# Kernel optimization log

Measured on AMD Instinct MI355X. Metric: run time of the kernel, lower is better.

Reference implementation:

```python
import jax, jax.numpy as jnp
import numpy as np

N = 4096      # number of projected gaussians
W = 512       # screen width
H = 512       # screen height
TL = 64       # tile_length
NT = W // TL  # tiles per axis (8) -> NT*NT = 64 tiles


def setup_inputs() -> dict:
    key = jax.random.key(0)
    k1, k2, k3, k4, k5 = jax.random.split(key, 5)
    xy = jax.random.uniform(k1, (N, 2), dtype=jnp.float32) * W          # screen positions
    depth = jax.random.uniform(k2, (N, 1), dtype=jnp.float32) * 10.0 + 0.1
    pos2d = jnp.concatenate([xy, depth], axis=1)                        # [N,3] = (x, y, depth)
    A = jax.random.normal(k3, (N, 2, 2), dtype=jnp.float32)
    cov2d = 9.0 * jnp.einsum('nij,nkj->nik', A, A) + jnp.eye(2, dtype=jnp.float32)  # PSD, ~3px sigma
    opacity = jax.random.uniform(k4, (N,), dtype=jnp.float32)
    color = jax.random.uniform(k5, (N, 3), dtype=jnp.float32)           # SH-evaluated RGB (pre +0.5 clamp)
    return {"pos2d": pos2d, "cov2d": cov2d, "opacity": opacity, "color": color}


def _render(pos2d, cov2d, opacity, color):
    # Global depth sort == per-tile argsort of the masked subset (order is preserved).
    order = jnp.argsort(pos2d[:, 2])
    pos = pos2d[order]
    cov = cov2d[order]
    op = opacity[order]
    col = jnp.clip(color[order] + 0.5, 0.0, None)  # color = clamp(eval_sh + 0.5, min=0)

    a, b = cov[:, 0, 0], cov[:, 0, 1]
    c, d = cov[:, 1, 0], cov[:, 1, 1]
    trace = a + d
    det = a * d - b * c
    term2 = 0.5 * jnp.sqrt(jnp.clip(trace * trace - 4.0 * det, 0.0, None))
    radius = 3.0 * jnp.sqrt(jnp.maximum(0.5 * trace - term2, 0.5 * trace + term2))

    inv_det = 1.0 / det
    ia = d * inv_det
    ib = -b * inv_det
    ic = -c * inv_det
    id_ = a * inv_det
    px, py = pos[:, 0], pos[:, 1]

    def tile_fn(tid):
        tx = tid // NT
        ty = tid % NT
        left = (tx * TL).astype(jnp.float32)
        top = (ty * TL).astype(jnp.float32)
        xs = left + jnp.arange(TL, dtype=jnp.float32)  # pixel x coords of tile rows
        ys = top + jnp.arange(TL, dtype=jnp.float32)   # pixel y coords of tile cols
        # gaussian's 3-sigma circle overlaps tile rect -> included in this tile
        inmask = ((px + radius >= left) & (px - radius < left + TL) &
                  (py + radius >= top) & (py - radius < top + TL))
        dx = xs[:, None, None] - px[None, None, :]  # [TL,1,K]
        dy = ys[None, :, None] - py[None, None, :]  # [1,TL,K]
        # mahalanobis distance: d^T Sigma^{-1} d  -> [TL,TL,K]
        q = ia * dx * dx + (ib + ic) * dx * dy + id_ * dy * dy
        prob = jnp.exp(-0.5 * q)
        alpha = jnp.where(inmask, jnp.clip(op * prob, 0.01, 0.99), 0.0)  # excluded -> alpha 0
        # transmittance: cumprod of (1 - alpha) shifted by one (front-to-back)
        ones = jnp.ones((TL, TL, 1), dtype=alpha.dtype)
        weight = jnp.cumprod(jnp.concatenate([ones, 1.0 - alpha[:, :, :-1]], axis=2), axis=2)
        return jnp.einsum('xyk,kc->xyc', alpha * weight, col)  # [TL,TL,3]

    tiles = jax.lax.map(tile_fn, jnp.arange(NT * NT))  # [NT*NT, TL, TL, 3]
    img = tiles.reshape(NT, NT, TL, TL, 3).transpose(0, 2, 1, 3, 4).reshape(W, H, 3)
    return img


def reference(pos2d, cov2d, opacity, color):
    return _render(pos2d, cov2d, opacity, color)
```

## Files before the change

kernel.cpp:

```cpp
#include <hip/hip_runtime.h>


#define N_G    4096
#define W_IMG  512
#define TL_    64
#define NTILES 64
#define LOG2E  1.44269504088896340736f

typedef float v2f __attribute__((ext_vector_type(2)));


__global__ __launch_bounds__(256)
void gs_preprocess(const float* __restrict__ pos2d,
                   const float* __restrict__ cov2d,
                   const float* __restrict__ opacity,
                   const float* __restrict__ color,
                   float4* __restrict__ a4,
                   float4* __restrict__ b4,
                   float* __restrict__ c1,
                   unsigned long long* __restrict__ tmask) {
    __shared__ __align__(16) float s_depth[N_G];
    const int t = threadIdx.x;

    for (int k = t; k < N_G; k += 256)
        s_depth[k] = pos2d[k * 3 + 2];
    __syncthreads();

    const int g = t >> 5;
    const int s = t & 31;
    const int i = blockIdx.x * 8 + g;
    const float di = s_depth[i];

    const float4* s_d4 = (const float4*)s_depth;
    int rank = 0;
    #pragma unroll 8
    for (int k = 0; k < 32; ++k) {
        const int j4 = s + 32 * k;
        const float4 d = s_d4[j4];
        const int j = 4 * j4;
        rank += (d.x < di) || (d.x == di && (j + 0) < i);
        rank += (d.y < di) || (d.y == di && (j + 1) < i);
        rank += (d.z < di) || (d.z == di && (j + 2) < i);
        rank += (d.w < di) || (d.w == di && (j + 3) < i);
    }
    rank += __shfl_xor(rank, 1);
    rank += __shfl_xor(rank, 2);
    rank += __shfl_xor(rank, 4);
    rank += __shfl_xor(rank, 8);
    rank += __shfl_xor(rank, 16);

    if (s == 0) {
        const float px = pos2d[i * 3 + 0];
        const float py = pos2d[i * 3 + 1];
        const float a = cov2d[i * 4 + 0];
        const float b = cov2d[i * 4 + 1];
        const float c = cov2d[i * 4 + 2];
        const float d = cov2d[i * 4 + 3];

        const float trace = a + d;
        const float det = a * d - b * c;
        const float tmp = trace * trace - 4.0f * det;
        const float term2 = 0.5f * sqrtf(fmaxf(tmp, 0.0f));
        const float radius = 3.0f * sqrtf(fmaxf(0.5f * trace - term2, 0.5f * trace + term2));
        const float inv_det = 1.0f / det;
        const float ia  = d * inv_det;
        const float ibc = (-b * inv_det) + (-c * inv_det);
        const float idd = a * inv_det;

        const float op = opacity[i];
        const float cr = fmaxf(color[i * 3 + 0] + 0.5f, 0.0f);
        const float cg = fmaxf(color[i * 3 + 1] + 0.5f, 0.0f);
        const float cb = fmaxf(color[i * 3 + 2] + 0.5f, 0.0f);

        unsigned int xm = 0, ym = 0;
        #pragma unroll
        for (int tc = 0; tc < 8; ++tc) {
            const float lo = (float)(tc * TL_);
            if ((px + radius >= lo) && (px - radius < lo + (float)TL_)) xm |= 1u << tc;
            if ((py + radius >= lo) && (py - radius < lo + (float)TL_)) ym |= 1u << tc;
        }
        unsigned long long m = 0ull;
        #pragma unroll
        for (int tc = 0; tc < 8; ++tc)
            if (xm & (1u << tc)) m |= (unsigned long long)ym << (8 * tc);

        a4[rank] = make_float4(px, py, -0.5f * ia * LOG2E, -0.5f * ibc * LOG2E);
        b4[rank] = make_float4(-0.5f * idd * LOG2E, __log2f(op), cr, cg);
        c1[rank] = cb;
        tmask[rank] = m;
    }
}

__global__ __launch_bounds__(512, 4)
void gs_render(const float4* __restrict__ a4,
               const float4* __restrict__ b4,
               const float* __restrict__ c1,
               const unsigned long long* __restrict__ tmask,
               float* __restrict__ out) {
    __shared__ unsigned short s_list[N_G];
    __shared__ int s_wcnt[8];
    __shared__ __align__(16) float4 s_wa[8][64];
    __shared__ __align__(16) float4 s_wb[8][64];
    __shared__ float s_wc[8][64];
    __shared__ __align__(16) float4 s_m[4][512];

    const int id = blockIdx.x;
    const int sub  = id >> 6;
    const int tile = ((id & 63) * 21 + sub * 11) & 63;
    const int tx = tile >> 3;
    const int ty = tile & 7;
    const int t = threadIdx.x;
    const int wave = t >> 6;
    const int lane = t & 63;

    unsigned int bits = 0;
    int wcnt = 0;
    #pragma unroll 4
    for (int it = 0; it < 8; ++it) {
        const int g = wave * 512 + it * 64 + lane;
        const bool m = (tmask[g] >> tile) & 1ull;
        bits |= (m ? 1u : 0u) << it;
        wcnt += __popcll(__ballot(m));
    }
    if (lane == 0) s_wcnt[wave] = wcnt;
    __syncthreads();
    int total = 0, base = 0;
    #pragma unroll
    for (int w = 0; w < 8; ++w) {
        const int c = s_wcnt[w];
        total += c;
        if (w < wave) base += c;
    }
    #pragma unroll 4
    for (int it = 0; it < 8; ++it) {
        const bool m = (bits >> it) & 1u;
        const unsigned long long bal = __ballot(m);
        const int prefix = __popcll(bal & ((1ULL << lane) - 1ULL));
        if (m) s_list[base + prefix] = (unsigned short)(wave * 512 + it * 64 + lane);
        base += __popcll(bal);
    }
    __syncthreads();

    const int s0 = (wave * total) >> 3;
    const int s1 = ((wave + 1) * total) >> 3;

    const int X0 = tx * TL_ + sub * 8;
    const int Y  = ty * TL_ + lane;
    const float fY = (float)Y;

    const v2f fX0 = {(float)(X0 + 0), (float)(X0 + 1)};
    const v2f fX1 = {(float)(X0 + 2), (float)(X0 + 3)};
    const v2f fX2 = {(float)(X0 + 4), (float)(X0 + 5)};
    const v2f fX3 = {(float)(X0 + 6), (float)(X0 + 7)};

    v2f R0 = {0.f, 0.f}, R1 = R0, R2 = R0, R3 = R0;
    v2f G0 = R0, G1 = R0, G2 = R0, G3 = R0;
    v2f B0 = R0, B1 = R0, B2 = R0, B3 = R0;
    v2f T0 = {1.f, 1.f}, T1 = T0, T2 = T0, T3 = T0;

    float4* const wa = s_wa[wave];
    float4* const wb = s_wb[wave];
    float*  const wc = s_wc[wave];

    float4 va, vb;
    float vc = 0.f;
    if (s0 + lane < s1) {
        const int g = s_list[s0 + lane];
        va = a4[g]; vb = b4[g]; vc = c1[g];
    }

    for (int c = s0; c < s1; c += 64) {
        const int n = min(64, s1 - c);
        if (lane < n) { wa[lane] = va; wb[lane] = vb; wc[lane] = vc; }
        const int cn = c + 64;
        if (cn + lane < s1) {
            const int g = s_list[cn + lane];
            va = a4[g]; vb = b4[g]; vc = c1[g];
        }
        #pragma unroll 4
        for (int k = 0; k < n; ++k) {
            const float4 A  = wa[k];
            const float4 Bv = wb[k];
            const float cbv = wc[k];

            const float dy   = fY - A.y;
            const float qbdy = A.w * dy;
            const float bse  = Bv.x * dy * dy + Bv.y;
            const v2f az2 = {A.z, A.z};
            const v2f ax2 = {A.x, A.x};
            const v2f qb2 = {qbdy, qbdy};
            const v2f bs2 = {bse, bse};
            const v2f lo2 = {0.01f, 0.01f};
            const v2f hi2 = {0.99f, 0.99f};
            const v2f cr2 = {Bv.z, Bv.z};
            const v2f cg2 = {Bv.w, Bv.w};
            const v2f cb2 = {cbv, cbv};
#define PX_PAIR(FXP, Tp, Rp, Gp, Bp)                                          \
            {                                                                 \
                const v2f dx = FXP - ax2;                                     \
                v2f q = __builtin_elementwise_fma(az2, dx, qb2);              \
                q = __builtin_elementwise_fma(q, dx, bs2);                    \
                v2f e;                                                        \
                e.x = exp2f(q.x); e.y = exp2f(q.y);                           \
                v2f al;                                                       \
                al.x = __builtin_amdgcn_fmed3f(e.x, lo2.x, hi2.x);            \
                al.y = __builtin_amdgcn_fmed3f(e.y, lo2.y, hi2.y);            \
                const v2f w_ = al * Tp;                                       \
                Rp = __builtin_elementwise_fma(w_, cr2, Rp);                  \
                Gp = __builtin_elementwise_fma(w_, cg2, Gp);                  \
                Bp = __builtin_elementwise_fma(w_, cb2, Bp);                  \
                Tp = Tp - w_;                                                 \
            }
            PX_PAIR(fX0, T0, R0, G0, B0)
            PX_PAIR(fX1, T1, R1, G1, B1)
            PX_PAIR(fX2, T2, R2, G2, B2)
            PX_PAIR(fX3, T3, R3, G3, B3)
#undef PX_PAIR
        }
    }

#define PUBLISH(buf)                                                          \
    {                                                                         \
        (buf)[0 * 64 + lane] = make_float4(R0.x, G0.x, B0.x, T0.x);           \
        (buf)[1 * 64 + lane] = make_float4(R0.y, G0.y, B0.y, T0.y);           \
        (buf)[2 * 64 + lane] = make_float4(R1.x, G1.x, B1.x, T1.x);           \
        (buf)[3 * 64 + lane] = make_float4(R1.y, G1.y, B1.y, T1.y);           \
        (buf)[4 * 64 + lane] = make_float4(R2.x, G2.x, B2.x, T2.x);           \
        (buf)[5 * 64 + lane] = make_float4(R2.y, G2.y, B2.y, T2.y);           \
        (buf)[6 * 64 + lane] = make_float4(R3.x, G3.x, B3.x, T3.x);           \
        (buf)[7 * 64 + lane] = make_float4(R3.y, G3.y, B3.y, T3.y);           \
    }
#define COMPOSE(buf)                                                          \
    {                                                                         \
        _Pragma("unroll")                                                     \
        for (int j = 0; j < 4; ++j) {                                         \
            const float4 m0 = (buf)[(2 * j + 0) * 64 + lane];                 \
            const float4 m1 = (buf)[(2 * j + 1) * 64 + lane];                 \
            const v2f mr = {m0.x, m1.x};                                      \
            const v2f mg = {m0.y, m1.y};                                      \
            const v2f mb = {m0.z, m1.z};                                      \
            const v2f mt = {m0.w, m1.w};                                      \
            v2f* Rj = j == 0 ? &R0 : j == 1 ? &R1 : j == 2 ? &R2 : &R3;       \
            v2f* Gj = j == 0 ? &G0 : j == 1 ? &G1 : j == 2 ? &G2 : &G3;       \
            v2f* Bj = j == 0 ? &B0 : j == 1 ? &B1 : j == 2 ? &B2 : &B3;       \
            v2f* Tj = j == 0 ? &T0 : j == 1 ? &T1 : j == 2 ? &T2 : &T3;       \
            *Rj = __builtin_elementwise_fma(*Tj, mr, *Rj);                    \
            *Gj = __builtin_elementwise_fma(*Tj, mg, *Gj);                    \
            *Bj = __builtin_elementwise_fma(*Tj, mb, *Bj);                    \
            *Tj = *Tj * mt;                                                   \
        }                                                                     \
    }

    if (wave & 1) PUBLISH(s_m[wave >> 1]);
    __syncthreads();
    if (!(wave & 1)) COMPOSE(s_m[wave >> 1]);
    if (wave == 2) PUBLISH(s_m[1]);
    if (wave == 6) PUBLISH(s_m[3]);
    __syncthreads();
    if (wave == 0) COMPOSE(s_m[1]);
    if (wave == 4) COMPOSE(s_m[3]);
    if (wave == 4) PUBLISH(s_m[3]);
    __syncthreads();
    if (wave == 0) {
        COMPOSE(s_m[3]);
#define OUT_PX(i, tv, rv, gv, bv)                                             \
        {                                                                     \
            const int o = ((X0 + (i)) * W_IMG + Y) * 3;                       \
            out[o + 0] = rv;                                                  \
            out[o + 1] = gv;                                                  \
            out[o + 2] = bv;                                                  \
        }
        OUT_PX(0, T0.x, R0.x, G0.x, B0.x)
        OUT_PX(1, T0.y, R0.y, G0.y, B0.y)
        OUT_PX(2, T1.x, R1.x, G1.x, B1.x)
        OUT_PX(3, T1.y, R1.y, G1.y, B1.y)
        OUT_PX(4, T2.x, R2.x, G2.x, B2.x)
        OUT_PX(5, T2.y, R2.y, G2.y, B2.y)
        OUT_PX(6, T3.x, R3.x, G3.x, B3.x)
        OUT_PX(7, T3.y, R3.y, G3.y, B3.y)
#undef OUT_PX
    }
#undef PUBLISH
#undef COMPOSE
}

extern "C" void kernel_launch(void* const* d_in, const int* in_sizes, int n_in,
                              void* d_out, int out_size, void* d_ws, size_t ws_size,
                              hipStream_t stream) {
    const float* pos2d   = (const float*)d_in[0];
    const float* cov2d   = (const float*)d_in[1];
    const float* opacity = (const float*)d_in[2];
    const float* color   = (const float*)d_in[3];
    float* out = (float*)d_out;

    char* ws = (char*)d_ws;
    float4* a4 = (float4*)(ws);
    float4* b4 = (float4*)(ws + 65536);
    float*  c1 = (float*)(ws + 131072);
    unsigned long long* tm = (unsigned long long*)(ws + 147456);

    gs_preprocess<<<N_G / 8, 256, 0, stream>>>(pos2d, cov2d, opacity, color,
                                               a4, b4, c1, tm);
    gs_render<<<NTILES * 8, 512, 0, stream>>>(a4, b4, c1, tm, out);
}
```

Baseline: 33.59 us.

## Schedule render blocks by per-tile gaussian count for load balancing

Preprocess now atomically counts the gaussians overlapping each tile. Every render block ranks the tiles by that count and remaps its block id so the heaviest tiles are dispatched first, with the sub-blocks interleaved to spread load. The aim is to cut the tail imbalance from uneven tile workloads. The cost is an extra memset launch, global atomics in preprocess, and a 64x64 ranking step repeated in every render block.

```diff
diff --git a/kernel.cpp b/kernel.cpp
--- a/kernel.cpp
+++ b/kernel.cpp
@@ -18,7 +18,8 @@
                    float4* __restrict__ a4,
                    float4* __restrict__ b4,
                    float* __restrict__ c1,
-                   unsigned long long* __restrict__ tmask) {
+                   unsigned long long* __restrict__ tmask,
+                   int* __restrict__ cnt) {
     __shared__ __align__(16) float s_depth[N_G];
     const int t = threadIdx.x;
 
@@ -88,6 +89,13 @@
         b4[rank] = make_float4(-0.5f * idd * LOG2E, __log2f(op), cr, cg);
         c1[rank] = cb;
         tmask[rank] = m;
+
+        unsigned long long mm = m;
+        while (mm) {
+            const int bit = (int)__builtin_ctzll(mm);
+            atomicAdd(&cnt[bit], 1);
+            mm &= mm - 1ull;
+        }
     }
 }
 
@@ -96,22 +104,42 @@
                const float4* __restrict__ b4,
                const float* __restrict__ c1,
                const unsigned long long* __restrict__ tmask,
+               const int* __restrict__ cnt,
                float* __restrict__ out) {
     __shared__ unsigned short s_list[N_G];
     __shared__ int s_wcnt[8];
+    __shared__ int s_cnt[64];
+    __shared__ unsigned char s_sorted[64];
     __shared__ __align__(16) float4 s_wa[8][64];
     __shared__ __align__(16) float4 s_wb[8][64];
     __shared__ float s_wc[8][64];
     __shared__ __align__(16) float4 s_m[4][512];
 
     const int id = blockIdx.x;
-    const int sub  = id >> 6;
-    const int tile = ((id & 63) * 21 + sub * 11) & 63;
-    const int tx = tile >> 3;
-    const int ty = tile & 7;
     const int t = threadIdx.x;
     const int wave = t >> 6;
     const int lane = t & 63;
+
+    if (t < 64) s_cnt[t] = cnt[t];
+    __syncthreads();
+    if (t < 64) {
+        const int c = s_cnt[t];
+        int r = 0;
+        #pragma unroll
+        for (int j = 0; j < 64; ++j) {
+            const int cj = s_cnt[j];
+            r += (cj > c) || (cj == c && j < t);
+        }
+        s_sorted[r] = (unsigned char)t;
+    }
+    __syncthreads();
+    const int slot = id & 63;
+    const int sub  = id >> 6;
+    const int rr = (sub < 4) ? ((slot + sub * 16) & 63)
+                             : (63 - ((slot + (sub - 4) * 16) & 63));
+    const int tile = s_sorted[rr];
+    const int tx = tile >> 3;
+    const int ty = tile & 7;
 
     unsigned int bits = 0;
     int wcnt = 0;
@@ -263,21 +291,21 @@
     __syncthreads();
     if (wave == 0) {
         COMPOSE(s_m[3]);
-#define OUT_PX(i, tv, rv, gv, bv)                                             \
+#define OUT_PX(i, rv, gv, bv)                                                 \
         {                                                                     \
             const int o = ((X0 + (i)) * W_IMG + Y) * 3;                       \
             out[o + 0] = rv;                                                  \
             out[o + 1] = gv;                                                  \
             out[o + 2] = bv;                                                  \
         }
-        OUT_PX(0, T0.x, R0.x, G0.x, B0.x)
-        OUT_PX(1, T0.y, R0.y, G0.y, B0.y)
-        OUT_PX(2, T1.x, R1.x, G1.x, B1.x)
-        OUT_PX(3, T1.y, R1.y, G1.y, B1.y)
-        OUT_PX(4, T2.x, R2.x, G2.x, B2.x)
-        OUT_PX(5, T2.y, R2.y, G2.y, B2.y)
-        OUT_PX(6, T3.x, R3.x, G3.x, B3.x)
-        OUT_PX(7, T3.y, R3.y, G3.y, B3.y)
+        OUT_PX(0, R0.x, G0.x, B0.x)
+        OUT_PX(1, R0.y, G0.y, B0.y)
+        OUT_PX(2, R1.x, G1.x, B1.x)
+        OUT_PX(3, R1.y, G1.y, B1.y)
+        OUT_PX(4, R2.x, G2.x, B2.x)
+        OUT_PX(5, R2.y, G2.y, B2.y)
+        OUT_PX(6, R3.x, G3.x, B3.x)
+        OUT_PX(7, R3.y, G3.y, B3.y)
 #undef OUT_PX
     }
 #undef PUBLISH
@@ -298,8 +326,10 @@
     float4* b4 = (float4*)(ws + 65536);
     float*  c1 = (float*)(ws + 131072);
     unsigned long long* tm = (unsigned long long*)(ws + 147456);
-
+    int*    ct = (int*)(ws + 180224);
+
+    hipMemsetAsync(ct, 0, 64 * sizeof(int), stream);
     gs_preprocess<<<N_G / 8, 256, 0, stream>>>(pos2d, cov2d, opacity, color,
-                                               a4, b4, c1, tm);
-    gs_render<<<NTILES * 8, 512, 0, stream>>>(a4, b4, c1, tm, out);
+                                               a4, b4, c1, tm, ct);
+    gs_render<<<NTILES * 8, 512, 0, stream>>>(a4, b4, c1, tm, ct, out);
 }
```

Result: slower. 72.43 us (+115.6%).

## Fuse preprocessing into render kernel with per-tile local depth sort

Applied to the files above, without the earlier changes.

Removes the separate preprocess kernel. Each render block now computes radii and tile overlap for all gaussians, sorts only the gaussians that touch its tile by a local rank count in shared memory, and builds its parameter arrays in LDS. The render loop reads those directly, replacing the chunked global-load double-buffering, and the final merge is serialized through two shared buffers. This saves a kernel launch and the global round-trip, but every block redundantly reads all 4096 gaussians, caps the per-tile list at 1024 entries, and adds more barriers to the merge.

```diff
diff --git a/kernel.cpp b/kernel.cpp
--- a/kernel.cpp
+++ b/kernel.cpp
@@ -5,120 +5,59 @@
 #define W_IMG  512
 #define TL_    64
 #define NTILES 64
+#define MAXG   1024
 #define LOG2E  1.44269504088896340736f
 
 typedef float v2f __attribute__((ext_vector_type(2)));
 
-
-__global__ __launch_bounds__(256)
-void gs_preprocess(const float* __restrict__ pos2d,
-                   const float* __restrict__ cov2d,
-                   const float* __restrict__ opacity,
-                   const float* __restrict__ color,
-                   float4* __restrict__ a4,
-                   float4* __restrict__ b4,
-                   float* __restrict__ c1,
-                   unsigned long long* __restrict__ tmask) {
-    __shared__ __align__(16) float s_depth[N_G];
-    const int t = threadIdx.x;
-
-    for (int k = t; k < N_G; k += 256)
-        s_depth[k] = pos2d[k * 3 + 2];
-    __syncthreads();
-
-    const int g = t >> 5;
-    const int s = t & 31;
-    const int i = blockIdx.x * 8 + g;
-    const float di = s_depth[i];
-
-    const float4* s_d4 = (const float4*)s_depth;
-    int rank = 0;
-    #pragma unroll 8
-    for (int k = 0; k < 32; ++k) {
-        const int j4 = s + 32 * k;
-        const float4 d = s_d4[j4];
-        const int j = 4 * j4;
-        rank += (d.x < di) || (d.x == di && (j + 0) < i);
-        rank += (d.y < di) || (d.y == di && (j + 1) < i);
-        rank += (d.z < di) || (d.z == di && (j + 2) < i);
-        rank += (d.w < di) || (d.w == di && (j + 3) < i);
-    }
-    rank += __shfl_xor(rank, 1);
-    rank += __shfl_xor(rank, 2);
-    rank += __shfl_xor(rank, 4);
-    rank += __shfl_xor(rank, 8);
-    rank += __shfl_xor(rank, 16);
-
-    if (s == 0) {
-        const float px = pos2d[i * 3 + 0];
-        const float py = pos2d[i * 3 + 1];
-        const float a = cov2d[i * 4 + 0];
-        const float b = cov2d[i * 4 + 1];
-        const float c = cov2d[i * 4 + 2];
-        const float d = cov2d[i * 4 + 3];
-
-        const float trace = a + d;
-        const float det = a * d - b * c;
-        const float tmp = trace * trace - 4.0f * det;
-        const float term2 = 0.5f * sqrtf(fmaxf(tmp, 0.0f));
-        const float radius = 3.0f * sqrtf(fmaxf(0.5f * trace - term2, 0.5f * trace + term2));
-        const float inv_det = 1.0f / det;
-        const float ia  = d * inv_det;
-        const float ibc = (-b * inv_det) + (-c * inv_det);
-        const float idd = a * inv_det;
-
-        const float op = opacity[i];
-        const float cr = fmaxf(color[i * 3 + 0] + 0.5f, 0.0f);
-        const float cg = fmaxf(color[i * 3 + 1] + 0.5f, 0.0f);
-        const float cb = fmaxf(color[i * 3 + 2] + 0.5f, 0.0f);
-
-        unsigned int xm = 0, ym = 0;
-        #pragma unroll
-        for (int tc = 0; tc < 8; ++tc) {
-            const float lo = (float)(tc * TL_);
-            if ((px + radius >= lo) && (px - radius < lo + (float)TL_)) xm |= 1u << tc;
-            if ((py + radius >= lo) && (py - radius < lo + (float)TL_)) ym |= 1u << tc;
-        }
-        unsigned long long m = 0ull;
-        #pragma unroll
-        for (int tc = 0; tc < 8; ++tc)
-            if (xm & (1u << tc)) m |= (unsigned long long)ym << (8 * tc);
-
-        a4[rank] = make_float4(px, py, -0.5f * ia * LOG2E, -0.5f * ibc * LOG2E);
-        b4[rank] = make_float4(-0.5f * idd * LOG2E, __log2f(op), cr, cg);
-        c1[rank] = cb;
-        tmask[rank] = m;
-    }
-}
+struct PreScratch {
+    float dep[MAXG];
+    unsigned short srv[MAXG];
+};
 
 __global__ __launch_bounds__(512, 4)
-void gs_render(const float4* __restrict__ a4,
-               const float4* __restrict__ b4,
-               const float* __restrict__ c1,
-               const unsigned long long* __restrict__ tmask,
-               float* __restrict__ out) {
-    __shared__ unsigned short s_list[N_G];
+void gs_fused(const float* __restrict__ pos2d,
+              const float* __restrict__ cov2d,
+              const float* __restrict__ opacity,
+              const float* __restrict__ color,
+              float* __restrict__ out) {
+    __shared__ __align__(16) float4 sA[MAXG];
+    __shared__ __align__(16) float4 sB[MAXG];
+    __shared__ float sC[MAXG];
     __shared__ int s_wcnt[8];
-    __shared__ __align__(16) float4 s_wa[8][64];
-    __shared__ __align__(16) float4 s_wb[8][64];
-    __shared__ float s_wc[8][64];
-    __shared__ __align__(16) float4 s_m[4][512];
+    __shared__ union {
+        PreScratch pre;
+        __align__(16) float4 m[2][512];
+    } su;
 
     const int id = blockIdx.x;
     const int sub  = id >> 6;
     const int tile = ((id & 63) * 21 + sub * 11) & 63;
     const int tx = tile >> 3;
     const int ty = tile & 7;
+    const float left = (float)(tx * TL_);
+    const float top  = (float)(ty * TL_);
     const int t = threadIdx.x;
     const int wave = t >> 6;
     const int lane = t & 63;
 
     unsigned int bits = 0;
     int wcnt = 0;
-    #pragma unroll 4
+    float dep8[8];
+    #pragma unroll
     for (int it = 0; it < 8; ++it) {
         const int g = wave * 512 + it * 64 + lane;
-        const bool m = (tmask[g] >> tile) & 1ull;
+        const float px = pos2d[g * 3 + 0];
+        const float py = pos2d[g * 3 + 1];
+        dep8[it] = pos2d[g * 3 + 2];
+        const float4 cv = ((const float4*)cov2d)[g];
+        const float trace = cv.x + cv.w;
+        const float det = cv.x * cv.w - cv.y * cv.z;
+        const float tmp = trace * trace - 4.0f * det;
+        const float term2 = 0.5f * sqrtf(fmaxf(tmp, 0.0f));
+        const float radius = 3.0f * sqrtf(fmaxf(0.5f * trace - term2, 0.5f * trace + term2));
+        const bool m = (px + radius >= left) && (px - radius < left + (float)TL_) &&
+                       (py + radius >= top)  && (py - radius < top  + (float)TL_);
         bits |= (m ? 1u : 0u) << it;
         wcnt += __popcll(__ballot(m));
     }
@@ -131,18 +70,63 @@
         total += c;
         if (w < wave) base += c;
     }
-    #pragma unroll 4
+    const int totalc = min(total, MAXG);
+
+    #pragma unroll
     for (int it = 0; it < 8; ++it) {
         const bool m = (bits >> it) & 1u;
         const unsigned long long bal = __ballot(m);
         const int prefix = __popcll(bal & ((1ULL << lane) - 1ULL));
-        if (m) s_list[base + prefix] = (unsigned short)(wave * 512 + it * 64 + lane);
+        const int pos = base + prefix;
+        if (m && pos < MAXG) {
+            su.pre.srv[pos] = (unsigned short)(wave * 512 + it * 64 + lane);
+            su.pre.dep[pos] = dep8[it];
+        }
         base += __popcll(bal);
     }
-    __syncthreads();
-
-    const int s0 = (wave * total) >> 3;
-    const int s1 = ((wave + 1) * total) >> 3;
+    if (t < 8) {
+        const int p = totalc + t;
+        if (p < MAXG) su.pre.dep[p] = 1e30f;
+    }
+    __syncthreads();
+
+    if (t < totalc) {
+        const float dt = su.pre.dep[t];
+        const float4* d4 = (const float4*)su.pre.dep;
+        int rank = 0;
+        const int n4 = (totalc + 3) >> 2;
+        for (int j4 = 0; j4 < n4; ++j4) {
+            const float4 d = d4[j4];
+            const int j = 4 * j4;
+            rank += (d.x < dt) || (d.x == dt && (j + 0) < t);
+            rank += (d.y < dt) || (d.y == dt && (j + 1) < t);
+            rank += (d.z < dt) || (d.z == dt && (j + 2) < t);
+            rank += (d.w < dt) || (d.w == dt && (j + 3) < t);
+        }
+        const int g = su.pre.srv[t];
+        const float px = pos2d[g * 3 + 0];
+        const float py = pos2d[g * 3 + 1];
+        const float a = cov2d[g * 4 + 0];
+        const float b = cov2d[g * 4 + 1];
+        const float c = cov2d[g * 4 + 2];
+        const float d = cov2d[g * 4 + 3];
+        const float det = a * d - b * c;
+        const float inv_det = 1.0f / det;
+        const float ia  = d * inv_det;
+        const float ibc = (-b * inv_det) + (-c * inv_det);
+        const float idd = a * inv_det;
+        const float op = opacity[g];
+        const float cr = fmaxf(color[g * 3 + 0] + 0.5f, 0.0f);
+        const float cg = fmaxf(color[g * 3 + 1] + 0.5f, 0.0f);
+        const float cb = fmaxf(color[g * 3 + 2] + 0.5f, 0.0f);
+        sA[rank] = make_float4(px, py, -0.5f * ia * LOG2E, -0.5f * ibc * LOG2E);
+        sB[rank] = make_float4(-0.5f * idd * LOG2E, __log2f(op), cr, cg);
+        sC[rank] = cb;
+    }
+    __syncthreads();
+
+    const int s0 = (wave * totalc) >> 3;
+    const int s1 = ((wave + 1) * totalc) >> 3;
 
     const int X0 = tx * TL_ + sub * 8;
     const int Y  = ty * TL_ + lane;
@@ -158,65 +142,45 @@
     v2f B0 = R0, B1 = R0, B2 = R0, B3 = R0;
     v2f T0 = {1.f, 1.f}, T1 = T0, T2 = T0, T3 = T0;
 
-    float4* const wa = s_wa[wave];
-    float4* const wb = s_wb[wave];
-    float*  const wc = s_wc[wave];
-
-    float4 va, vb;
-    float vc = 0.f;
-    if (s0 + lane < s1) {
-        const int g = s_list[s0 + lane];
-        va = a4[g]; vb = b4[g]; vc = c1[g];
-    }
-
-    for (int c = s0; c < s1; c += 64) {
-        const int n = min(64, s1 - c);
-        if (lane < n) { wa[lane] = va; wb[lane] = vb; wc[lane] = vc; }
-        const int cn = c + 64;
-        if (cn + lane < s1) {
-            const int g = s_list[cn + lane];
-            va = a4[g]; vb = b4[g]; vc = c1[g];
-        }
-        #pragma unroll 4
-        for (int k = 0; k < n; ++k) {
-            const float4 A  = wa[k];
-            const float4 Bv = wb[k];
-            const float cbv = wc[k];
-
-            const float dy   = fY - A.y;
-            const float qbdy = A.w * dy;
-            const float bse  = Bv.x * dy * dy + Bv.y;
-            const v2f az2 = {A.z, A.z};
-            const v2f ax2 = {A.x, A.x};
-            const v2f qb2 = {qbdy, qbdy};
-            const v2f bs2 = {bse, bse};
-            const v2f lo2 = {0.01f, 0.01f};
-            const v2f hi2 = {0.99f, 0.99f};
-            const v2f cr2 = {Bv.z, Bv.z};
-            const v2f cg2 = {Bv.w, Bv.w};
-            const v2f cb2 = {cbv, cbv};
+    #pragma unroll 4
+    for (int k = s0; k < s1; ++k) {
+        const float4 A  = sA[k];
+        const float4 Bv = sB[k];
+        const float cbv = sC[k];
+
+        const float dy   = fY - A.y;
+        const float qbdy = A.w * dy;
+        const float bse  = Bv.x * dy * dy + Bv.y;
+        const v2f az2 = {A.z, A.z};
+        const v2f ax2 = {A.x, A.x};
+        const v2f qb2 = {qbdy, qbdy};
+        const v2f bs2 = {bse, bse};
+        const v2f lo2 = {0.01f, 0.01f};
+        const v2f hi2 = {0.99f, 0.99f};
+        const v2f cr2 = {Bv.z, Bv.z};
+        const v2f cg2 = {Bv.w, Bv.w};
+        const v2f cb2 = {cbv, cbv};
 #define PX_PAIR(FXP, Tp, Rp, Gp, Bp)                                          \
-            {                                                                 \
-                const v2f dx = FXP - ax2;                                     \
-                v2f q = __builtin_elementwise_fma(az2, dx, qb2);              \
-                q = __builtin_elementwise_fma(q, dx, bs2);                    \
-                v2f e;                                                        \
-                e.x = exp2f(q.x); e.y = exp2f(q.y);                           \
-                v2f al;                                                       \
-                al.x = __builtin_amdgcn_fmed3f(e.x, lo2.x, hi2.x);            \
-                al.y = __builtin_amdgcn_fmed3f(e.y, lo2.y, hi2.y);            \
-                const v2f w_ = al * Tp;                                       \
-                Rp = __builtin_elementwise_fma(w_, cr2, Rp);                  \
-                Gp = __builtin_elementwise_fma(w_, cg2, Gp);                  \
-                Bp = __builtin_elementwise_fma(w_, cb2, Bp);                  \
-                Tp = Tp - w_;                                                 \
-            }
-            PX_PAIR(fX0, T0, R0, G0, B0)
-            PX_PAIR(fX1, T1, R1, G1, B1)
-            PX_PAIR(fX2, T2, R2, G2, B2)
-            PX_PAIR(fX3, T3, R3, G3, B3)
+        {                                                                     \
+            const v2f dx = FXP - ax2;                                         \
+            v2f q = __builtin_elementwise_fma(az2, dx, qb2);                  \
+            q = __builtin_elementwise_fma(q, dx, bs2);                        \
+            v2f e;                                                            \
+            e.x = exp2f(q.x); e.y = exp2f(q.y);                               \
+            v2f al;                                                           \
+            al.x = __builtin_amdgcn_fmed3f(e.x, lo2.x, hi2.x);                \
+            al.y = __builtin_amdgcn_fmed3f(e.y, lo2.y, hi2.y);                \
+            const v2f w_ = al * Tp;                                           \
+            Rp = __builtin_elementwise_fma(w_, cr2, Rp);                      \
+            Gp = __builtin_elementwise_fma(w_, cg2, Gp);                      \
+            Bp = __builtin_elementwise_fma(w_, cb2, Bp);                      \
+            Tp = Tp - w_;                                                     \
+        }
+        PX_PAIR(fX0, T0, R0, G0, B0)
+        PX_PAIR(fX1, T1, R1, G1, B1)
+        PX_PAIR(fX2, T2, R2, G2, B2)
+        PX_PAIR(fX3, T3, R3, G3, B3)
 #undef PX_PAIR
-        }
     }
 
 #define PUBLISH(buf)                                                          \
@@ -251,33 +215,43 @@
         }                                                                     \
     }
 
-    if (wave & 1) PUBLISH(s_m[wave >> 1]);
-    __syncthreads();
-    if (!(wave & 1)) COMPOSE(s_m[wave >> 1]);
-    if (wave == 2) PUBLISH(s_m[1]);
-    if (wave == 6) PUBLISH(s_m[3]);
-    __syncthreads();
-    if (wave == 0) COMPOSE(s_m[1]);
-    if (wave == 4) COMPOSE(s_m[3]);
-    if (wave == 4) PUBLISH(s_m[3]);
+    if (wave == 1) PUBLISH(su.m[0]);
+    if (wave == 3) PUBLISH(su.m[1]);
+    __syncthreads();
+    if (wave == 0) COMPOSE(su.m[0]);
+    if (wave == 2) COMPOSE(su.m[1]);
+    __syncthreads();
+    if (wave == 5) PUBLISH(su.m[0]);
+    if (wave == 7) PUBLISH(su.m[1]);
+    __syncthreads();
+    if (wave == 4) COMPOSE(su.m[0]);
+    if (wave == 6) COMPOSE(su.m[1]);
+    __syncthreads();
+    if (wave == 2) PUBLISH(su.m[0]);
+    if (wave == 6) PUBLISH(su.m[1]);
+    __syncthreads();
+    if (wave == 0) COMPOSE(su.m[0]);
+    if (wave == 4) COMPOSE(su.m[1]);
+    __syncthreads();
+    if (wave == 4) PUBLISH(su.m[0]);
     __syncthreads();
     if (wave == 0) {
-        COMPOSE(s_m[3]);
-#define OUT_PX(i, tv, rv, gv, bv)                                             \
+        COMPOSE(su.m[0]);
+#define OUT_PX(i, rv, gv, bv)                                                 \
         {                                                                     \
             const int o = ((X0 + (i)) * W_IMG + Y) * 3;                       \
             out[o + 0] = rv;                                                  \
             out[o + 1] = gv;                                                  \
             out[o + 2] = bv;                                                  \
         }
-        OUT_PX(0, T0.x, R0.x, G0.x, B0.x)
-        OUT_PX(1, T0.y, R0.y, G0.y, B0.y)
-        OUT_PX(2, T1.x, R1.x, G1.x, B1.x)
-        OUT_PX(3, T1.y, R1.y, G1.y, B1.y)
-        OUT_PX(4, T2.x, R2.x, G2.x, B2.x)
-        OUT_PX(5, T2.y, R2.y, G2.y, B2.y)
-        OUT_PX(6, T3.x, R3.x, G3.x, B3.x)
-        OUT_PX(7, T3.y, R3.y, G3.y, B3.y)
+        OUT_PX(0, R0.x, G0.x, B0.x)
+        OUT_PX(1, R0.y, G0.y, B0.y)
+        OUT_PX(2, R1.x, G1.x, B1.x)
+        OUT_PX(3, R1.y, G1.y, B1.y)
+        OUT_PX(4, R2.x, G2.x, B2.x)
+        OUT_PX(5, R2.y, G2.y, B2.y)
+        OUT_PX(6, R3.x, G3.x, B3.x)
+        OUT_PX(7, R3.y, G3.y, B3.y)
 #undef OUT_PX
     }
 #undef PUBLISH
@@ -293,13 +267,5 @@
     const float* color   = (const float*)d_in[3];
     float* out = (float*)d_out;
 
-    char* ws = (char*)d_ws;
-    float4* a4 = (float4*)(ws);
-    float4* b4 = (float4*)(ws + 65536);
-    float*  c1 = (float*)(ws + 131072);
-    unsigned long long* tm = (unsigned long long*)(ws + 147456);
-
-    gs_preprocess<<<N_G / 8, 256, 0, stream>>>(pos2d, cov2d, opacity, color,
-                                               a4, b4, c1, tm);
-    gs_render<<<NTILES * 8, 512, 0, stream>>>(a4, b4, c1, tm, out);
+    gs_fused<<<NTILES * 8, 512, 0, stream>>>(pos2d, cov2d, opacity, color, out);
 }
```

New measurement: 31.91 us. 1.05x faster.
